# Kernel tuning notes

Hardware: AMD Instinct MI355X
Metric: run time of the kernel (lower is better)

## Reference

```python
import jax, jax.numpy as jnp
import numpy as np

V, E, H, L = 32000, 512, 1024, 2
B, S = 16, 128


def _gru_cell(x, h, w_ih, w_hh, b_ih, b_hh):
    # PyTorch GRUCell: gates ordered (r, z, n), chunks of size H
    gi = x @ w_ih.T + b_ih            # (B, 3H)
    gh = h @ w_hh.T + b_hh            # (B, 3H)
    i_r, i_z, i_n = jnp.split(gi, 3, axis=-1)
    h_r, h_z, h_n = jnp.split(gh, 3, axis=-1)
    r = jax.nn.sigmoid(i_r + h_r)
    z = jax.nn.sigmoid(i_z + h_z)
    n = jnp.tanh(i_n + r * h_n)
    return (1.0 - z) * n + z * h


def setup_inputs() -> dict:
    key = jax.random.key(0)
    ks = jax.random.split(key, 16)
    s = lambda fan: 1.0 / np.sqrt(fan)
    inp = {
        "hidden": jax.random.normal(ks[0], (L, B, H), jnp.float32),
        "trg": jax.random.randint(ks[1], (B, S), 0, V),
        "embedding": jax.random.normal(ks[2], (V, E), jnp.float32) * 0.02,
        # layer 0 GRU (input_size=E)
        "w_ih0": jax.random.uniform(ks[3], (3 * H, E), jnp.float32, -s(H), s(H)),
        "w_hh0": jax.random.uniform(ks[4], (3 * H, H), jnp.float32, -s(H), s(H)),
        "b_ih0": jnp.zeros((3 * H,), jnp.float32),
        "b_hh0": jnp.zeros((3 * H,), jnp.float32),
        # layer 1 GRU (input_size=H)
        "w_ih1": jax.random.uniform(ks[5], (3 * H, H), jnp.float32, -s(H), s(H)),
        "w_hh1": jax.random.uniform(ks[6], (3 * H, H), jnp.float32, -s(H), s(H)),
        "b_ih1": jnp.zeros((3 * H,), jnp.float32),
        "b_hh1": jnp.zeros((3 * H,), jnp.float32),
        # output projection MLP: Linear(H,H) -> ReLU -> Linear(H,E)
        "w1": jax.random.uniform(ks[7], (H, H), jnp.float32, -s(H), s(H)),
        "b1": jnp.zeros((H,), jnp.float32),
        "w2": jax.random.uniform(ks[8], (E, H), jnp.float32, -s(H), s(H)),
        "b2": jnp.zeros((E,), jnp.float32),
        # generator bias (weight tied to embedding)
        "b_gen": jnp.zeros((V,), jnp.float32),
    }
    return inp


def reference(hidden, trg, embedding, w_ih0, w_hh0, b_ih0, b_hh0,
              w_ih1, w_hh1, b_ih1, b_hh1, w1, b1, w2, b2, b_gen):
    def step(h, tok):
        # h: (L, B, H); tok: (B,)
        x = embedding[tok]                                 # (B, E)
        h0 = _gru_cell(x, h[0], w_ih0, w_hh0, b_ih0, b_hh0)
        h1 = _gru_cell(h0, h[1], w_ih1, w_hh1, b_ih1, b_hh1)
        new_h = jnp.stack([h0, h1], axis=0)
        out = jax.nn.relu(h1 @ w1.T + b1) @ w2.T + b2      # (B, E)
        logit = out @ embedding.T + b_gen                  # (B, V) weight-tied
        return new_h, logit

    _, logits = jax.lax.scan(step, hidden, trg.T)          # (S, B, V)
    return jnp.transpose(logits, (1, 0, 2))                # (B, S, V)
```

## Files before the change

### kernel.cpp

```cpp
#include <hip/hip_runtime.h>
#include <math.h>

#define Sn 128
#define Bn 16
#define Hn 1024
#define En 512
#define Vn 32000
#define H3 3072
#define NL0 32
#define NL1 64

typedef _Float16 h16;
typedef __attribute__((ext_vector_type(4))) _Float16 h16x4;
typedef __attribute__((ext_vector_type(8))) _Float16 h16x8;
typedef __attribute__((ext_vector_type(4))) float f32x4;

#define Q_EMB   4096000
#define Q_WIH0  (Q_EMB + 393216)
#define Q_W1    (Q_WIH0 + 262144)
#define Q_W2    (Q_W1 + 131072)
#define Q_WHH0  (Q_W2 + 786432)
#define Q_WIH1  (Q_WHH0 + 786432)
#define Q_WHH1  (Q_WIH1 + 786432)
#define Q_HID   (Q_WHH1 + 8192)
__global__ __launch_bounds__(256) void cvt_all_k(
    const float* __restrict__ emb, const float* __restrict__ wih0,
    const float* __restrict__ w1, const float* __restrict__ w2,
    const float* __restrict__ whh0, const float* __restrict__ wih1,
    const float* __restrict__ whh1, const float* __restrict__ hid,
    h16* __restrict__ E, h16* __restrict__ A, h16* __restrict__ B1,
    h16* __restrict__ B2, h16* __restrict__ D0, h16* __restrict__ D1,
    h16* __restrict__ D2, h16* __restrict__ HD)
{
  int i = blockIdx.x * 256 + threadIdx.x;
  const float* s; h16* d; int o;
  if      (i < Q_EMB)  { s = emb;  d = E;  o = i; }
  else if (i < Q_WIH0) { s = wih0; d = A;  o = i - Q_EMB; }
  else if (i < Q_W1)   { s = w1;   d = B1; o = i - Q_WIH0; }
  else if (i < Q_W2)   { s = w2;   d = B2; o = i - Q_W1; }
  else if (i < Q_WHH0) { s = whh0; d = D0; o = i - Q_W2; }
  else if (i < Q_WIH1) { s = wih1; d = D1; o = i - Q_WHH0; }
  else if (i < Q_WHH1) { s = whh1; d = D2; o = i - Q_WIH1; }
  else                 { s = hid;  d = HD; o = i - Q_WHH1; }
  float4 v = *(const float4*)(s + (size_t)o * 4);
  h16x4 ov = { (h16)v.x, (h16)v.y, (h16)v.z, (h16)v.w };
  *(h16x4*)(d + (size_t)o * 4) = ov;
}

__global__ void embed_k(const int* __restrict__ trg, const float* __restrict__ emb,
                        h16* __restrict__ Xh) {
  int t = blockIdx.x;
  int s = t >> 4, b = t & 15;
  int tok = trg[b * Sn + s];
  const float* src = emb + (size_t)tok * En;
  int e = threadIdx.x * 4;
  float4 v = *(const float4*)(src + e);
  h16x4 o = { (h16)v.x, (h16)v.y, (h16)v.z, (h16)v.w };
  *(h16x4*)(Xh + (size_t)t * En + e) = o;
}

template<int OUT_MODE, bool RELU, bool SWZ>
__global__ __launch_bounds__(256) void gemm_bt(
    const h16* __restrict__ A, const h16* __restrict__ B,
    const float* __restrict__ bias, void* __restrict__ C,
    int M, int N, int K)
{
  __shared__ h16 As[128 * 64];
  __shared__ h16 Bs[128 * 64];
  int tid = threadIdx.x;
  int l = tid & 63, wv = tid >> 6;
  int wr = wv >> 1, wc = wv & 1;

  int work = blockIdx.x;
  if (SWZ) { int q = gridDim.x >> 3; work = (work & 7) * q + (work >> 3); }
  int nMp = M >> 7;
  int brow = (work % nMp) << 7;
  int bcol = (work / nMp) << 7;

  f32x4 acc[4][4];
#pragma unroll
  for (int m = 0; m < 4; ++m)
#pragma unroll
    for (int n = 0; n < 4; ++n) acc[m][n] = (f32x4){0.f, 0.f, 0.f, 0.f};

  int nkt = K >> 6;
  for (int kt = 0; kt < nkt; ++kt) {
    const h16* Ag = A + (size_t)brow * K + kt * 64;
    const h16* Bg = B + (size_t)bcol * K + kt * 64;
#pragma unroll
    for (int c = tid; c < 2048; c += 256) {
      int half = c >> 10;
      int cc = c & 1023;
      int row = cc >> 3, slot = cc & 7;
      const h16* src = (half ? Bg : Ag) + (size_t)row * K + slot * 8;
      uint4 v = *(const uint4*)src;
      h16* dst = (half ? Bs : As) + row * 64 + ((slot ^ (row & 7)) << 3);
      *(uint4*)dst = v;
    }
    __syncthreads();
#pragma unroll
    for (int kk = 0; kk < 2; ++kk) {
      h16x8 af[4], bfr[4];
      int rb = wr * 64 + (l & 15);
      int cb2 = wc * 64 + (l & 15);
      int slot = kk * 4 + (l >> 4);
#pragma unroll
      for (int m = 0; m < 4; ++m) {
        int r = rb + m * 16;
        af[m] = *(const h16x8*)&As[r * 64 + ((slot ^ (r & 7)) << 3)];
      }
#pragma unroll
      for (int n = 0; n < 4; ++n) {
        int r = cb2 + n * 16;
        bfr[n] = *(const h16x8*)&Bs[r * 64 + ((slot ^ (r & 7)) << 3)];
      }
#pragma unroll
      for (int m = 0; m < 4; ++m)
#pragma unroll
        for (int n = 0; n < 4; ++n)
          acc[m][n] = __builtin_amdgcn_mfma_f32_16x16x32_f16(af[m], bfr[n], acc[m][n], 0, 0, 0);
    }
    __syncthreads();
  }

#pragma unroll
  for (int m = 0; m < 4; ++m) {
    int row0 = brow + wr * 64 + m * 16 + ((l >> 4) << 2);
#pragma unroll
    for (int n = 0; n < 4; ++n) {
      int col = bcol + wc * 64 + n * 16 + (l & 15);
      float bv = bias ? bias[col] : 0.f;
#pragma unroll
      for (int i = 0; i < 4; ++i) {
        int row = row0 + i;
        float v = acc[m][n][i] + bv;
        if (RELU) v = fmaxf(v, 0.f);
        if (OUT_MODE == 1) {
          ((h16*)C)[(size_t)row * N + col] = (h16)v;
        } else {
          ((float*)C)[(size_t)row * N + col] = v;
        }
      }
    }
  }
}


__device__ __forceinline__ void wait_fL1(int* fL1, int target, int tid) {
  if (tid < 64) {
    for (;;) {
      int v = __hip_atomic_load(&fL1[tid << 5], __ATOMIC_RELAXED, __HIP_MEMORY_SCOPE_AGENT);
      if (__all(v >= target)) break;
      __builtin_amdgcn_s_sleep(8);
    }
  }
  __syncthreads();
  asm volatile("" ::: "memory");
}

__device__ __forceinline__ void wait_cnt(int* c, int target, int tid) {
  if (tid == 0) {
    while (__hip_atomic_load(c, __ATOMIC_RELAXED, __HIP_MEMORY_SCOPE_AGENT) < target)
      __builtin_amdgcn_s_sleep(8);
  }
  __syncthreads();
  asm volatile("" ::: "memory");
}

__device__ __forceinline__ void publish_cnt(int* c) {
  __syncthreads();
  if (threadIdx.x == 0) {
    __threadfence();
    atomicAdd(c, 1);
  }
}

__device__ __forceinline__ void gemm_head128(
    const h16* __restrict__ A, const h16* __restrict__ B, const float* __restrict__ bias,
    h16* __restrict__ C, int ldc, int K, int relu, char* dyn, int tid)
{
  h16* As = (h16*)dyn;
  h16* Bs = (h16*)(dyn + 16384);
  int l = tid & 63, wv = tid >> 6;
  int wr = wv >> 1, wc = wv & 1;
  f32x4 acc[4][4];
#pragma unroll
  for (int m = 0; m < 4; ++m)
#pragma unroll
    for (int n = 0; n < 4; ++n) acc[m][n] = (f32x4){0.f, 0.f, 0.f, 0.f};
  int nkt = K >> 6;
  for (int kt = 0; kt < nkt; ++kt) {
    const h16* Ag = A + kt * 64;
    const h16* Bg = B + kt * 64;
    for (int c = tid; c < 2048; c += 384) {
      int half = c >> 10, cc = c & 1023, row = cc >> 3, slot = cc & 7;
      const h16* src = (half ? Bg : Ag) + (size_t)row * K + slot * 8;
      uint4 v = *(const uint4*)src;
      h16* dst = (half ? Bs : As) + row * 64 + ((slot ^ (row & 7)) << 3);
      *(uint4*)dst = v;
    }
    __syncthreads();
    if (wv < 4) {
#pragma unroll
      for (int kk = 0; kk < 2; ++kk) {
        h16x8 af[4], bfr[4];
        int rb = wr * 64 + (l & 15);
        int cb2 = wc * 64 + (l & 15);
        int slot = kk * 4 + (l >> 4);
#pragma unroll
        for (int m = 0; m < 4; ++m) {
          int r = rb + m * 16;
          af[m] = *(const h16x8*)&As[r * 64 + ((slot ^ (r & 7)) << 3)];
        }
#pragma unroll
        for (int n = 0; n < 4; ++n) {
          int r = cb2 + n * 16;
          bfr[n] = *(const h16x8*)&Bs[r * 64 + ((slot ^ (r & 7)) << 3)];
        }
#pragma unroll
        for (int m = 0; m < 4; ++m)
#pragma unroll
          for (int n = 0; n < 4; ++n)
            acc[m][n] = __builtin_amdgcn_mfma_f32_16x16x32_f16(af[m], bfr[n], acc[m][n], 0, 0, 0);
      }
    }
    __syncthreads();
  }
  if (wv < 4) {
#pragma unroll
    for (int m = 0; m < 4; ++m) {
      int row0 = wr * 64 + m * 16 + ((l >> 4) << 2);
#pragma unroll
      for (int n = 0; n < 4; ++n) {
        int col = wc * 64 + n * 16 + (l & 15);
        float bv = bias[col];
#pragma unroll
        for (int i = 0; i < 4; ++i) {
          float v = acc[m][n][i] + bv;
          if (relu) v = fmaxf(v, 0.f);
          C[(size_t)(row0 + i) * ldc + col] = (h16)v;
        }
      }
    }
  }
}

__device__ __forceinline__ void gemm_headlogit(
    const h16* __restrict__ A, const h16* __restrict__ B, const float* __restrict__ bias,
    float* __restrict__ C, int growbase, char* dyn, int tid)
{
  h16* As = (h16*)dyn;
  h16* Bs = (h16*)(dyn + 16384);
  int l = tid & 63, wv = tid >> 6;
  int wr = wv >> 1, wc = wv & 1;
  f32x4 acc[4][8];
#pragma unroll
  for (int m = 0; m < 4; ++m)
#pragma unroll
    for (int n = 0; n < 8; ++n) acc[m][n] = (f32x4){0.f, 0.f, 0.f, 0.f};
  for (int kt = 0; kt < 8; ++kt) {
    const h16* Ag = A + kt * 64;
    const h16* Bg = B + kt * 64;
    for (int c = tid; c < 3072; c += 384) {
      int isB = (c >= 1024);
      int cc = isB ? (c - 1024) : c;
      int row = cc >> 3, slot = cc & 7;
      const h16* src = (isB ? Bg : Ag) + (size_t)row * 512 + slot * 8;
      uint4 v = *(const uint4*)src;
      h16* dst = (isB ? Bs : As) + row * 64 + ((slot ^ (row & 7)) << 3);
      *(uint4*)dst = v;
    }
    __syncthreads();
    if (wv < 4) {
#pragma unroll
      for (int kk = 0; kk < 2; ++kk) {
        h16x8 af[4], bfr[8];
        int rb = wr * 64 + (l & 15);
        int cb2 = wc * 128 + (l & 15);
        int slot = kk * 4 + (l >> 4);
#pragma unroll
        for (int m = 0; m < 4; ++m) {
          int r = rb + m * 16;
          af[m] = *(const h16x8*)&As[r * 64 + ((slot ^ (r & 7)) << 3)];
        }
#pragma unroll
        for (int n = 0; n < 8; ++n) {
          int r = cb2 + n * 16;
          bfr[n] = *(const h16x8*)&Bs[r * 64 + ((slot ^ (r & 7)) << 3)];
        }
#pragma unroll
        for (int m = 0; m < 4; ++m)
#pragma unroll
          for (int n = 0; n < 8; ++n)
            acc[m][n] = __builtin_amdgcn_mfma_f32_16x16x32_f16(af[m], bfr[n], acc[m][n], 0, 0, 0);
      }
    }
    __syncthreads();
  }
  if (wv < 4) {
#pragma unroll
    for (int m = 0; m < 4; ++m) {
      int row0 = wr * 64 + m * 16 + ((l >> 4) << 2);
#pragma unroll
      for (int n = 0; n < 8; ++n) {
        int col = wc * 128 + n * 16 + (l & 15);
        float bv = bias[col];
#pragma unroll
        for (int i = 0; i < 4; ++i) {
          int grow = growbase + row0 + i;
          int rr = ((grow & 15) << 7) + (grow >> 4);
          C[(size_t)rr * Vn + col] = acc[m][n][i] + bv;
        }
      }
    }
  }
}

__global__ __launch_bounds__(384) void mega(
    const float* __restrict__ gi0,
    const float* __restrict__ hidden,
    const h16* __restrict__ hinit16,
    const h16* __restrict__ whh0, const float* __restrict__ bhh0,
    const h16* __restrict__ wih1, const float* __restrict__ bih1,
    const h16* __restrict__ whh1, const float* __restrict__ bhh1,
    h16* __restrict__ h0ring, h16* __restrict__ H1A,
    int* __restrict__ flags,
    const h16* __restrict__ w1H, const float* __restrict__ b1, h16* __restrict__ Tb,
    const h16* __restrict__ w2H, const float* __restrict__ b2, h16* __restrict__ Ub,
    const h16* __restrict__ embH, const float* __restrict__ b_gen,
    float* __restrict__ out)
{
  extern __shared__ char dyn[];
  int bid = blockIdx.x;
  int tid = threadIdx.x;

  __threadfence();

  int* fL0  = flags;
  int* fL1  = flags + 1024;
  int* cnt1 = flags + 3072;
  int* cnt2 = flags + 3328;

  if (bid < NL0 + NL1) {
    float* exch = (float*)dyn;
    int w = tid >> 6, l = tid & 63;
    int li = l & 15;
    int ko = (l >> 4) << 3;
    int b0 = (l >> 4) << 2;

    if (bid < NL0) {
      int gate = w >> 1, ch = w & 1;
      int j = bid * 32 + ch * 16 + li;
      h16x8 Bf[32];
      {
        const h16* wp = whh0 + ((size_t)((gate << 10) + j) << 10) + ko;
#pragma unroll
        for (int t = 0; t < 32; ++t) Bf[t] = *(const h16x8*)(wp + t * 32);
      }
      float bR = 0.f, bZ = 0.f, bN = 0.f;
      float hprev[4];
      if (gate == 2) {
        bR = bhh0[j]; bZ = bhh0[1024 + j]; bN = bhh0[2048 + j];
#pragma unroll
        for (int i = 0; i < 4; ++i) hprev[i] = hidden[((b0 + i) << 10) + j];
      }
      for (int s = 0; s < Sn; ++s) {
        if (s > 0) {
          if (w == 0 && l < NL0)
            while (__hip_atomic_load(&fL0[l << 5], __ATOMIC_RELAXED, __HIP_MEMORY_SCOPE_AGENT) < s) {}
          __syncthreads();
          asm volatile("" ::: "memory");
        }
        float gr[4], gz[4], gn[4];
        if (gate == 2) {
          const float* gb = gi0 + ((size_t)s << 4) * H3;
#pragma unroll
          for (int i = 0; i < 4; ++i) {
            const float* g = gb + (size_t)(b0 + i) * H3 + j;
            gr[i] = g[0]; gz[i] = g[1024]; gn[i] = g[2048];
          }
        }
        const h16* hsrc = (s == 0) ? hinit16 : h0ring + (((size_t)(s - 1)) << 14);
        const h16* Ap = hsrc + (li << 10) + ko;
        f32x4 acc = (f32x4){0.f, 0.f, 0.f, 0.f};
#pragma unroll
        for (int t = 0; t < 32; ++t)
          acc = __builtin_amdgcn_mfma_f32_16x16x32_f16(*(const h16x8*)(Ap + t * 32), Bf[t], acc, 0, 0, 0);
        if (w < 4) {
#pragma unroll
          for (int i = 0; i < 4; ++i) exch[w * 256 + ((b0 + i) << 4) + li] = acc[i];
        }
        __syncthreads();
        if (gate == 2) {
#pragma unroll
          for (int i = 0; i < 4; ++i) {
            int e = ((b0 + i) << 4) + li;
            float r = 1.f / (1.f + expf(-(exch[ch * 256 + e] + bR + gr[i])));
            float z = 1.f / (1.f + expf(-(exch[(2 + ch) * 256 + e] + bZ + gz[i])));
            float n = tanhf(gn[i] + r * (acc[i] + bN));
            float o = (1.f - z) * n + z * hprev[i];
            hprev[i] = o;
            h16 hv = (h16)o; unsigned short us; __builtin_memcpy(&us, &hv, 2);
            __hip_atomic_store((unsigned short*)h0ring + (((size_t)s) << 14) + ((b0 + i) << 10) + j,
                               us, __ATOMIC_RELAXED, __HIP_MEMORY_SCOPE_AGENT);
          }
        }
        __syncthreads();
        if (tid == 0)
          __hip_atomic_store(&fL0[bid << 5], s + 1, __ATOMIC_RELAXED, __HIP_MEMORY_SCOPE_AGENT);
      }
    } else {
      int bl = bid - NL0;
      int j = (bl << 4) + li;
      int isHH = (w >= 3);
      int gate = isHH ? (w - 3) : w;
      h16x8 Bf[32];
      {
        const h16* wsrc = isHH ? whh1 : wih1;
        const h16* wp = wsrc + ((size_t)((gate << 10) + j) << 10) + ko;
#pragma unroll
        for (int t = 0; t < 32; ++t) Bf[t] = *(const h16x8*)(wp + t * 32);
      }
      float bIR = 0.f, bIZ = 0.f, bIN = 0.f, bHR = 0.f, bHZ = 0.f, bHN = 0.f;
      float hprev[4];
      if (w == 5) {
        bIR = bih1[j]; bIZ = bih1[1024 + j]; bIN = bih1[2048 + j];
        bHR = bhh1[j]; bHZ = bhh1[1024 + j]; bHN = bhh1[2048 + j];
#pragma unroll
        for (int i = 0; i < 4; ++i) hprev[i] = hidden[16384 + ((b0 + i) << 10) + j];
      }
      for (int s = 1; s <= Sn; ++s) {
        if (w == 0) {
          if (l < NL0)
            while (__hip_atomic_load(&fL0[l << 5], __ATOMIC_RELAXED, __HIP_MEMORY_SCOPE_AGENT) < s) {}
        } else if (w == 1 && s >= 2) {
          while (__hip_atomic_load(&fL1[l << 5], __ATOMIC_RELAXED, __HIP_MEMORY_SCOPE_AGENT) < s) {}
        }
        __syncthreads();
        asm volatile("" ::: "memory");
        const h16* hsrc = isHH
            ? ((s == 1) ? hinit16 + 16384 : H1A + (((size_t)(s - 2)) << 14))
            : (h0ring + (((size_t)(s - 1)) << 14));
        const h16* Ap = hsrc + (li << 10) + ko;
        f32x4 acc = (f32x4){0.f, 0.f, 0.f, 0.f};
#pragma unroll
        for (int t = 0; t < 32; ++t)
          acc = __builtin_amdgcn_mfma_f32_16x16x32_f16(*(const h16x8*)(Ap + t * 32), Bf[t], acc, 0, 0, 0);
        if (w < 5) {
#pragma unroll
          for (int i = 0; i < 4; ++i) exch[w * 256 + ((b0 + i) << 4) + li] = acc[i];
        }
        __syncthreads();
        if (w == 5) {
#pragma unroll
          for (int i = 0; i < 4; ++i) {
            int e = ((b0 + i) << 4) + li;
            float r = 1.f / (1.f + expf(-(exch[e] + bIR + exch[768 + e] + bHR)));
            float z = 1.f / (1.f + expf(-(exch[256 + e] + bIZ + exch[1024 + e] + bHZ)));
            float n = tanhf(exch[512 + e] + bIN + r * (acc[i] + bHN));
            float o = (1.f - z) * n + z * hprev[i];
            hprev[i] = o;
            h16 hv = (h16)o; unsigned short us; __builtin_memcpy(&us, &hv, 2);
            __hip_atomic_store((unsigned short*)H1A + (((size_t)(s - 1)) << 14) + ((b0 + i) << 10) + j,
                               us, __ATOMIC_RELAXED, __HIP_MEMORY_SCOPE_AGENT);
          }
        }
        __syncthreads();
        if (tid == 0)
          __hip_atomic_store(&fL1[bl << 5], s + 1, __ATOMIC_RELAXED, __HIP_MEMORY_SCOPE_AGENT);
      }
    }
    return;
  }

  int hb = bid - (NL0 + NL1);
  int m = hb / 137;
  int r = hb - m * 137;

  if (r < 8) {
    wait_fL1(fL1, 8 * m + 9, tid);
    gemm_head128(H1A + (size_t)(m * 128) * Hn, w1H + (size_t)(r * 128) * Hn,
                 b1 + r * 128, Tb + (size_t)(m * 128) * Hn + r * 128, Hn, Hn, 1, dyn, tid);
    publish_cnt(&cnt1[m << 3]);
  } else if (r < 12) {
    int rn = r - 8;
    wait_cnt(&cnt1[m << 3], 8, tid);
    gemm_head128(Tb + (size_t)(m * 128) * Hn, w2H + (size_t)(rn * 128) * Hn,
                 b2 + rn * 128, Ub + (size_t)(m * 128) * En + rn * 128, En, Hn, 0, dyn, tid);
    publish_cnt(&cnt2[m << 3]);
  } else {
    int np = r - 12;
    wait_cnt(&cnt2[m << 3], 4, tid);
    gemm_headlogit(Ub + (size_t)(m * 128) * En, embH + (size_t)(np * 256) * En,
                   b_gen + np * 256, out + np * 256, m * 128, dyn, tid);
  }
}

extern "C" void kernel_launch(void* const* d_in, const int* in_sizes, int n_in,
                              void* d_out, int out_size, void* d_ws, size_t ws_size,
                              hipStream_t stream) {
  const float* hidden = (const float*)d_in[0];
  const int*   trg    = (const int*)d_in[1];
  const float* emb    = (const float*)d_in[2];
  const float* w_ih0  = (const float*)d_in[3];
  const float* w_hh0  = (const float*)d_in[4];
  const float* b_ih0  = (const float*)d_in[5];
  const float* b_hh0  = (const float*)d_in[6];
  const float* w_ih1  = (const float*)d_in[7];
  const float* w_hh1  = (const float*)d_in[8];
  const float* b_ih1  = (const float*)d_in[9];
  const float* b_hh1  = (const float*)d_in[10];
  const float* w1     = (const float*)d_in[11];
  const float* b1     = (const float*)d_in[12];
  const float* w2     = (const float*)d_in[13];
  const float* b2     = (const float*)d_in[14];
  const float* b_gen  = (const float*)d_in[15];

  char* ws = (char*)d_ws;
  size_t off = 0;
  float* GI0    = (float*)(ws + off); off += (size_t)Sn * Bn * H3 * 4;
  h16* Xh       = (h16*)(ws + off);   off += (size_t)Sn * Bn * En * 2;
  h16* embH     = (h16*)(ws + off);   off += (size_t)Vn * En * 2;
  h16* wih0H    = (h16*)(ws + off);   off += (size_t)H3 * En * 2;
  h16* w1H      = (h16*)(ws + off);   off += (size_t)Hn * Hn * 2;
  h16* w2H      = (h16*)(ws + off);   off += (size_t)En * Hn * 2;
  h16* whh0H    = (h16*)(ws + off);   off += (size_t)H3 * Hn * 2;
  h16* wih1H    = (h16*)(ws + off);   off += (size_t)H3 * Hn * 2;
  h16* whh1H    = (h16*)(ws + off);   off += (size_t)H3 * Hn * 2;
  h16* H1A      = (h16*)(ws + off);   off += (size_t)Sn * Bn * Hn * 2;
  h16* h0ring   = (h16*)(ws + off);   off += (size_t)Sn * Bn * Hn * 2;
  h16* hinit16  = (h16*)(ws + off);   off += (size_t)2 * Bn * Hn * 2;
  h16* Tb       = (h16*)(ws + off);   off += (size_t)Sn * Bn * Hn * 2;
  h16* Ub       = (h16*)(ws + off);   off += (size_t)Sn * Bn * En * 2;
  int* flags    = (int*)(ws + off);   off += 16384;

  cvt_all_k<<<28320, 256, 0, stream>>>(emb, w_ih0, w1, w2, w_hh0, w_ih1, w_hh1, hidden,
                                       embH, wih0H, w1H, w2H, whh0H, wih1H, whh1H, hinit16);
  embed_k<<<Sn * Bn, 128, 0, stream>>>(trg, emb, Xh);

  gemm_bt<0, false, true><<<384, 256, 0, stream>>>(Xh, wih0H, b_ih0, GI0, Sn * Bn, H3, En);

  (void)hipMemsetAsync(flags, 0, 16384, stream);
  const int LDSZ = 49152;
  (void)hipFuncSetAttribute(reinterpret_cast<const void*>(mega),
                            hipFuncAttributeMaxDynamicSharedMemorySize, LDSZ);
  mega<<<NL0 + NL1 + 16 * 137, 384, LDSZ, stream>>>(
      GI0, hidden, hinit16, whh0H, b_hh0, wih1H, b_ih1, whh1H, b_hh1,
      h0ring, H1A, flags, w1H, b1, Tb, w2H, b2, Ub, embH, b_gen, (float*)d_out);
}
```

Before: 1.373 ms.

## Fold input-projection GEMM into persistent kernel and make head blocks loop over chunks

Drops the separate gi0 GEMM launch and runs it as 384 extra blocks inside the persistent kernel. Layer-0 recurrent blocks now wait on per-chunk counters, so the recurrence can start before all of gi0 is computed. The recurrent weight fp16 conversion moves out of the cvt kernel: the recurrent blocks convert fp32 weights into registers as they load them. The head blocks shrink from 16×137 to 137 persistent blocks, each looping over 16 row chunks. The cost is that fewer head blocks now serialize the chunks, and correctness depends on all blocks being co-resident so the spin waits cannot deadlock.

```diff
diff --git a/kernel.cpp b/kernel.cpp
--- a/kernel.cpp
+++ b/kernel.cpp
@@ -9,6 +9,7 @@
 #define H3 3072
 #define NL0 32
 #define NL1 64
+#define NGI 384
 
 typedef _Float16 h16;
 typedef __attribute__((ext_vector_type(4))) _Float16 h16x4;
@@ -19,29 +20,22 @@
 #define Q_WIH0  (Q_EMB + 393216)
 #define Q_W1    (Q_WIH0 + 262144)
 #define Q_W2    (Q_W1 + 131072)
-#define Q_WHH0  (Q_W2 + 786432)
-#define Q_WIH1  (Q_WHH0 + 786432)
-#define Q_WHH1  (Q_WIH1 + 786432)
-#define Q_HID   (Q_WHH1 + 8192)
+#define Q_HID   (Q_W2 + 8192)
 __global__ __launch_bounds__(256) void cvt_all_k(
     const float* __restrict__ emb, const float* __restrict__ wih0,
     const float* __restrict__ w1, const float* __restrict__ w2,
-    const float* __restrict__ whh0, const float* __restrict__ wih1,
-    const float* __restrict__ whh1, const float* __restrict__ hid,
+    const float* __restrict__ hid,
     h16* __restrict__ E, h16* __restrict__ A, h16* __restrict__ B1,
-    h16* __restrict__ B2, h16* __restrict__ D0, h16* __restrict__ D1,
-    h16* __restrict__ D2, h16* __restrict__ HD)
+    h16* __restrict__ B2, h16* __restrict__ HD)
 {
   int i = blockIdx.x * 256 + threadIdx.x;
+  if (i >= Q_HID) return;
   const float* s; h16* d; int o;
   if      (i < Q_EMB)  { s = emb;  d = E;  o = i; }
   else if (i < Q_WIH0) { s = wih0; d = A;  o = i - Q_EMB; }
   else if (i < Q_W1)   { s = w1;   d = B1; o = i - Q_WIH0; }
   else if (i < Q_W2)   { s = w2;   d = B2; o = i - Q_W1; }
-  else if (i < Q_WHH0) { s = whh0; d = D0; o = i - Q_W2; }
-  else if (i < Q_WIH1) { s = wih1; d = D1; o = i - Q_WHH0; }
-  else if (i < Q_WHH1) { s = whh1; d = D2; o = i - Q_WIH1; }
-  else                 { s = hid;  d = HD; o = i - Q_WHH1; }
+  else                 { s = hid;  d = HD; o = i - Q_W2; }
   float4 v = *(const float4*)(s + (size_t)o * 4);
   h16x4 ov = { (h16)v.x, (h16)v.y, (h16)v.z, (h16)v.w };
   *(h16x4*)(d + (size_t)o * 4) = ov;
@@ -59,92 +53,6 @@
   *(h16x4*)(Xh + (size_t)t * En + e) = o;
 }
 
-template<int OUT_MODE, bool RELU, bool SWZ>
-__global__ __launch_bounds__(256) void gemm_bt(
-    const h16* __restrict__ A, const h16* __restrict__ B,
-    const float* __restrict__ bias, void* __restrict__ C,
-    int M, int N, int K)
-{
-  __shared__ h16 As[128 * 64];
-  __shared__ h16 Bs[128 * 64];
-  int tid = threadIdx.x;
-  int l = tid & 63, wv = tid >> 6;
-  int wr = wv >> 1, wc = wv & 1;
-
-  int work = blockIdx.x;
-  if (SWZ) { int q = gridDim.x >> 3; work = (work & 7) * q + (work >> 3); }
-  int nMp = M >> 7;
-  int brow = (work % nMp) << 7;
-  int bcol = (work / nMp) << 7;
-
-  f32x4 acc[4][4];
-#pragma unroll
-  for (int m = 0; m < 4; ++m)
-#pragma unroll
-    for (int n = 0; n < 4; ++n) acc[m][n] = (f32x4){0.f, 0.f, 0.f, 0.f};
-
-  int nkt = K >> 6;
-  for (int kt = 0; kt < nkt; ++kt) {
-    const h16* Ag = A + (size_t)brow * K + kt * 64;
-    const h16* Bg = B + (size_t)bcol * K + kt * 64;
-#pragma unroll
-    for (int c = tid; c < 2048; c += 256) {
-      int half = c >> 10;
-      int cc = c & 1023;
-      int row = cc >> 3, slot = cc & 7;
-      const h16* src = (half ? Bg : Ag) + (size_t)row * K + slot * 8;
-      uint4 v = *(const uint4*)src;
-      h16* dst = (half ? Bs : As) + row * 64 + ((slot ^ (row & 7)) << 3);
-      *(uint4*)dst = v;
-    }
-    __syncthreads();
-#pragma unroll
-    for (int kk = 0; kk < 2; ++kk) {
-      h16x8 af[4], bfr[4];
-      int rb = wr * 64 + (l & 15);
-      int cb2 = wc * 64 + (l & 15);
-      int slot = kk * 4 + (l >> 4);
-#pragma unroll
-      for (int m = 0; m < 4; ++m) {
-        int r = rb + m * 16;
-        af[m] = *(const h16x8*)&As[r * 64 + ((slot ^ (r & 7)) << 3)];
-      }
-#pragma unroll
-      for (int n = 0; n < 4; ++n) {
-        int r = cb2 + n * 16;
-        bfr[n] = *(const h16x8*)&Bs[r * 64 + ((slot ^ (r & 7)) << 3)];
-      }
-#pragma unroll
-      for (int m = 0; m < 4; ++m)
-#pragma unroll
-        for (int n = 0; n < 4; ++n)
-          acc[m][n] = __builtin_amdgcn_mfma_f32_16x16x32_f16(af[m], bfr[n], acc[m][n], 0, 0, 0);
-    }
-    __syncthreads();
-  }
-
-#pragma unroll
-  for (int m = 0; m < 4; ++m) {
-    int row0 = brow + wr * 64 + m * 16 + ((l >> 4) << 2);
-#pragma unroll
-    for (int n = 0; n < 4; ++n) {
-      int col = bcol + wc * 64 + n * 16 + (l & 15);
-      float bv = bias ? bias[col] : 0.f;
-#pragma unroll
-      for (int i = 0; i < 4; ++i) {
-        int row = row0 + i;
-        float v = acc[m][n][i] + bv;
-        if (RELU) v = fmaxf(v, 0.f);
-        if (OUT_MODE == 1) {
-          ((h16*)C)[(size_t)row * N + col] = (h16)v;
-        } else {
-          ((float*)C)[(size_t)row * N + col] = v;
-        }
-      }
-    }
-  }
-}
-
 
 __device__ __forceinline__ void wait_fL1(int* fL1, int target, int tid) {
   if (tid < 64) {
@@ -175,9 +83,10 @@
   }
 }
 
-__device__ __forceinline__ void gemm_head128(
+template<int OUTF32>
+__device__ __forceinline__ void gemm_t128(
     const h16* __restrict__ A, const h16* __restrict__ B, const float* __restrict__ bias,
-    h16* __restrict__ C, int ldc, int K, int relu, char* dyn, int tid)
+    void* __restrict__ C, int ldc, int K, int relu, char* dyn, int tid)
 {
   h16* As = (h16*)dyn;
   h16* Bs = (h16*)(dyn + 16384);
@@ -238,7 +147,8 @@
         for (int i = 0; i < 4; ++i) {
           float v = acc[m][n][i] + bv;
           if (relu) v = fmaxf(v, 0.f);
-          C[(size_t)(row0 + i) * ldc + col] = (h16)v;
+          if (OUTF32) ((float*)C)[(size_t)(row0 + i) * ldc + col] = v;
+          else        ((h16*)C)[(size_t)(row0 + i) * ldc + col] = (h16)v;
         }
       }
     }
@@ -320,11 +230,12 @@
     const float* __restrict__ gi0,
     const float* __restrict__ hidden,
     const h16* __restrict__ hinit16,
-    const h16* __restrict__ whh0, const float* __restrict__ bhh0,
-    const h16* __restrict__ wih1, const float* __restrict__ bih1,
-    const h16* __restrict__ whh1, const float* __restrict__ bhh1,
+    const float* __restrict__ whh0, const float* __restrict__ bhh0,
+    const float* __restrict__ wih1, const float* __restrict__ bih1,
+    const float* __restrict__ whh1, const float* __restrict__ bhh1,
     h16* __restrict__ h0ring, h16* __restrict__ H1A,
     int* __restrict__ flags,
+    const h16* __restrict__ Xh, const h16* __restrict__ wih0H, const float* __restrict__ b_ih0,
     const h16* __restrict__ w1H, const float* __restrict__ b1, h16* __restrict__ Tb,
     const h16* __restrict__ w2H, const float* __restrict__ b2, h16* __restrict__ Ub,
     const h16* __restrict__ embH, const float* __restrict__ b_gen,
@@ -336,10 +247,11 @@
 
   __threadfence();
 
-  int* fL0  = flags;
-  int* fL1  = flags + 1024;
-  int* cnt1 = flags + 3072;
-  int* cnt2 = flags + 3328;
+  int* fL0   = flags;
+  int* fL1   = flags + 1024;
+  int* cnt1  = flags + 3072;
+  int* cnt2  = flags + 3328;
+  int* cntGI = flags + 3584;
 
   if (bid < NL0 + NL1) {
     float* exch = (float*)dyn;
@@ -353,9 +265,15 @@
       int j = bid * 32 + ch * 16 + li;
       h16x8 Bf[32];
       {
-        const h16* wp = whh0 + ((size_t)((gate << 10) + j) << 10) + ko;
-#pragma unroll
-        for (int t = 0; t < 32; ++t) Bf[t] = *(const h16x8*)(wp + t * 32);
+        const float* wp = whh0 + ((size_t)((gate << 10) + j) << 10) + ko;
+#pragma unroll
+        for (int t = 0; t < 32; ++t) {
+          float4 u0 = *(const float4*)(wp + t * 32);
+          float4 u1 = *(const float4*)(wp + t * 32 + 4);
+          h16x8 f = { (h16)u0.x, (h16)u0.y, (h16)u0.z, (h16)u0.w,
+                      (h16)u1.x, (h16)u1.y, (h16)u1.z, (h16)u1.w };
+          Bf[t] = f;
+        }
       }
       float bR = 0.f, bZ = 0.f, bN = 0.f;
       float hprev[4];
@@ -365,12 +283,14 @@
         for (int i = 0; i < 4; ++i) hprev[i] = hidden[((b0 + i) << 10) + j];
       }
       for (int s = 0; s < Sn; ++s) {
-        if (s > 0) {
-          if (w == 0 && l < NL0)
+        if (w == 0) {
+          if (l < NL0 && s > 0)
             while (__hip_atomic_load(&fL0[l << 5], __ATOMIC_RELAXED, __HIP_MEMORY_SCOPE_AGENT) < s) {}
-          __syncthreads();
-          asm volatile("" ::: "memory");
-        }
+          if (l == 32)
+            while (__hip_atomic_load(&cntGI[(s >> 3) << 3], __ATOMIC_RELAXED, __HIP_MEMORY_SCOPE_AGENT) < 24) {}
+        }
+        __syncthreads();
+        asm volatile("" ::: "memory");
         float gr[4], gz[4], gn[4];
         if (gate == 2) {
           const float* gb = gi0 + ((size_t)s << 4) * H3;
@@ -416,10 +336,16 @@
       int gate = isHH ? (w - 3) : w;
       h16x8 Bf[32];
       {
-        const h16* wsrc = isHH ? whh1 : wih1;
-        const h16* wp = wsrc + ((size_t)((gate << 10) + j) << 10) + ko;
-#pragma unroll
-        for (int t = 0; t < 32; ++t) Bf[t] = *(const h16x8*)(wp + t * 32);
+        const float* wsrc = isHH ? whh1 : wih1;
+        const float* wp = wsrc + ((size_t)((gate << 10) + j) << 10) + ko;
+#pragma unroll
+        for (int t = 0; t < 32; ++t) {
+          float4 u0 = *(const float4*)(wp + t * 32);
+          float4 u1 = *(const float4*)(wp + t * 32 + 4);
+          h16x8 f = { (h16)u0.x, (h16)u0.y, (h16)u0.z, (h16)u0.w,
+                      (h16)u1.x, (h16)u1.y, (h16)u1.z, (h16)u1.w };
+          Bf[t] = f;
+        }
       }
       float bIR = 0.f, bIZ = 0.f, bIN = 0.f, bHR = 0.f, bHZ = 0.f, bHN = 0.f;
       float hprev[4];
@@ -474,25 +400,40 @@
   }
 
   int hb = bid - (NL0 + NL1);
-  int m = hb / 137;
-  int r = hb - m * 137;
-
-  if (r < 8) {
-    wait_fL1(fL1, 8 * m + 9, tid);
-    gemm_head128(H1A + (size_t)(m * 128) * Hn, w1H + (size_t)(r * 128) * Hn,
-                 b1 + r * 128, Tb + (size_t)(m * 128) * Hn + r * 128, Hn, Hn, 1, dyn, tid);
-    publish_cnt(&cnt1[m << 3]);
-  } else if (r < 12) {
-    int rn = r - 8;
-    wait_cnt(&cnt1[m << 3], 8, tid);
-    gemm_head128(Tb + (size_t)(m * 128) * Hn, w2H + (size_t)(rn * 128) * Hn,
-                 b2 + rn * 128, Ub + (size_t)(m * 128) * En + rn * 128, En, Hn, 0, dyn, tid);
-    publish_cnt(&cnt2[m << 3]);
+
+  if (hb < NGI) {
+    int p = hb / 24, n = hb % 24;
+    gemm_t128<1>(Xh + (size_t)(p * 128) * En, wih0H + (size_t)(n * 128) * En,
+                 b_ih0 + n * 128, (float*)gi0 + (size_t)(p * 128) * H3 + n * 128,
+                 H3, En, 0, dyn, tid);
+    publish_cnt(&cntGI[p << 3]);
+    return;
+  }
+
+  int hh = hb - NGI;
+  if (hh < 8) {
+    int r = hh;
+    for (int m = 0; m < 16; ++m) {
+      wait_fL1(fL1, 8 * m + 9, tid);
+      gemm_t128<0>(H1A + (size_t)(m * 128) * Hn, w1H + (size_t)(r * 128) * Hn,
+                   b1 + r * 128, Tb + (size_t)(m * 128) * Hn + r * 128, Hn, Hn, 1, dyn, tid);
+      publish_cnt(&cnt1[m << 3]);
+    }
+  } else if (hh < 12) {
+    int rn = hh - 8;
+    for (int m = 0; m < 16; ++m) {
+      wait_cnt(&cnt1[m << 3], 8, tid);
+      gemm_t128<0>(Tb + (size_t)(m * 128) * Hn, w2H + (size_t)(rn * 128) * Hn,
+                   b2 + rn * 128, Ub + (size_t)(m * 128) * En + rn * 128, En, Hn, 0, dyn, tid);
+      publish_cnt(&cnt2[m << 3]);
+    }
   } else {
-    int np = r - 12;
-    wait_cnt(&cnt2[m << 3], 4, tid);
-    gemm_headlogit(Ub + (size_t)(m * 128) * En, embH + (size_t)(np * 256) * En,
-                   b_gen + np * 256, out + np * 256, m * 128, dyn, tid);
+    int np = hh - 12;
+    for (int m = 0; m < 16; ++m) {
+      wait_cnt(&cnt2[m << 3], 4, tid);
+      gemm_headlogit(Ub + (size_t)(m * 128) * En, embH + (size_t)(np * 256) * En,
+                     b_gen + np * 256, out + np * 256, m * 128, dyn, tid);
+    }
   }
 }
 
@@ -524,9 +465,6 @@
   h16* wih0H    = (h16*)(ws + off);   off += (size_t)H3 * En * 2;
   h16* w1H      = (h16*)(ws + off);   off += (size_t)Hn * Hn * 2;
   h16* w2H      = (h16*)(ws + off);   off += (size_t)En * Hn * 2;
-  h16* whh0H    = (h16*)(ws + off);   off += (size_t)H3 * Hn * 2;
-  h16* wih1H    = (h16*)(ws + off);   off += (size_t)H3 * Hn * 2;
-  h16* whh1H    = (h16*)(ws + off);   off += (size_t)H3 * Hn * 2;
   h16* H1A      = (h16*)(ws + off);   off += (size_t)Sn * Bn * Hn * 2;
   h16* h0ring   = (h16*)(ws + off);   off += (size_t)Sn * Bn * Hn * 2;
   h16* hinit16  = (h16*)(ws + off);   off += (size_t)2 * Bn * Hn * 2;
@@ -534,17 +472,16 @@
   h16* Ub       = (h16*)(ws + off);   off += (size_t)Sn * Bn * En * 2;
   int* flags    = (int*)(ws + off);   off += 16384;
 
-  cvt_all_k<<<28320, 256, 0, stream>>>(emb, w_ih0, w1, w2, w_hh0, w_ih1, w_hh1, hidden,
-                                       embH, wih0H, w1H, w2H, whh0H, wih1H, whh1H, hinit16);
+  cvt_all_k<<<19104, 256, 0, stream>>>(emb, w_ih0, w1, w2, hidden,
+                                       embH, wih0H, w1H, w2H, hinit16);
   embed_k<<<Sn * Bn, 128, 0, stream>>>(trg, emb, Xh);
-
-  gemm_bt<0, false, true><<<384, 256, 0, stream>>>(Xh, wih0H, b_ih0, GI0, Sn * Bn, H3, En);
 
   (void)hipMemsetAsync(flags, 0, 16384, stream);
   const int LDSZ = 49152;
   (void)hipFuncSetAttribute(reinterpret_cast<const void*>(mega),
                             hipFuncAttributeMaxDynamicSharedMemorySize, LDSZ);
-  mega<<<NL0 + NL1 + 16 * 137, 384, LDSZ, stream>>>(
-      GI0, hidden, hinit16, whh0H, b_hh0, wih1H, b_ih1, whh1H, b_hh1,
-      h0ring, H1A, flags, w1H, b1, Tb, w2H, b2, Ub, embH, b_gen, (float*)d_out);
-}
+  mega<<<NL0 + NL1 + NGI + 137, 384, LDSZ, stream>>>(
+      GI0, hidden, hinit16, w_hh0, b_hh0, w_ih1, b_ih1, w_hh1, b_hh1,
+      h0ring, H1A, flags, Xh, wih0H, b_ih0, w1H, b1, Tb, w2H, b2, Ub,
+      embH, b_gen, (float*)d_out);
+}
```

New measurement: 1.233 ms. -10.2%, faster.
